# Kernel tuning notes

Measured on AMD Instinct MI355X. Metric: run time of the kernel, lower is better.

## Reference

```python
import jax, jax.numpy as jnp
import numpy as np

D_MODEL = 1024
N_HEADS = 16
HEAD_DIM = D_MODEL // N_HEADS
B, LQ, LK = 2, 2048, 2048
NEG_BIG = -1.0e9


def setup_inputs() -> dict:
    key = jax.random.key(0)
    ks = jax.random.split(key, 12)
    s = 1.0 / np.sqrt(D_MODEL)
    inp = {
        "query": jax.random.normal(ks[0], (B, LQ, D_MODEL), jnp.float32),
        "key": jax.random.normal(ks[1], (B, LK, D_MODEL), jnp.float32),
        "value": jax.random.normal(ks[2], (B, LK, D_MODEL), jnp.float32),
        "mask": jax.random.randint(ks[3], (B, 1, 1, LK), 0, 2, jnp.int32),
        "Wq": jax.random.normal(ks[4], (D_MODEL, D_MODEL), jnp.float32) * s,
        "bq": jnp.zeros((D_MODEL,), jnp.float32),
        "Wk": jax.random.normal(ks[5], (D_MODEL, D_MODEL), jnp.float32) * s,
        "bk": jnp.zeros((D_MODEL,), jnp.float32),
        "Wv": jax.random.normal(ks[6], (D_MODEL, D_MODEL), jnp.float32) * s,
        "bv": jnp.zeros((D_MODEL,), jnp.float32),
        "Wo": jax.random.normal(ks[7], (D_MODEL, D_MODEL), jnp.float32) * s,
        "bo": jnp.zeros((D_MODEL,), jnp.float32),
    }
    return inp


def _split_heads(x):
    # (B, L, E) -> (B, H, L, Dh)
    b, l, _ = x.shape
    return x.reshape(b, l, N_HEADS, HEAD_DIM).transpose(0, 2, 1, 3)


def reference(query, key, value, mask, Wq, bq, Wk, bk, Wv, bv, Wo, bo):
    q = _split_heads(query @ Wq + bq)   # (B,H,Lq,Dh)
    k = _split_heads(key @ Wk + bk)     # (B,H,Lk,Dh)
    v = _split_heads(value @ Wv + bv)   # (B,H,Lk,Dh)

    scale = 1.0 / jnp.sqrt(jnp.asarray(HEAD_DIM, jnp.float32))
    scores = jnp.einsum("bhqd,bhkd->bhqk", q, k) * scale
    scores = scores + mask.astype(scores.dtype) * NEG_BIG
    attn_weights = jax.nn.softmax(scores, axis=-1)  # (B,H,Lq,Lk)
    # dropout in inference mode -> identity
    attn_out = jnp.einsum("bhqk,bhkd->bhqd", attn_weights, v)
    attn_out = attn_out.transpose(0, 2, 1, 3).reshape(B, LQ, D_MODEL)
    out = attn_out @ Wo + bo  # output dropout is identity at inference
    return out, attn_weights
```

## Files before the change

### kernel.cpp

```cpp
#include <hip/hip_runtime.h>


typedef unsigned short u16;
typedef __attribute__((ext_vector_type(8))) short s16x8;
typedef __attribute__((ext_vector_type(8))) unsigned short u16x8;
typedef __attribute__((ext_vector_type(4))) float f32x4;

__device__ __forceinline__ u16 f2b(float f) {
  union { float f; unsigned u; } v; v.f = f;
  return (u16)((v.u + 0x7FFFu + ((v.u >> 16) & 1u)) >> 16);
}

__global__ void cvt_kernel(const float* __restrict__ src, u16* __restrict__ dst, int n8) {
  int i = blockIdx.x * 256 + threadIdx.x;
  if (i >= n8) return;
  typedef __attribute__((ext_vector_type(4))) float f4;
  f4 a = ((const f4*)src)[2 * i];
  f4 b = ((const f4*)src)[2 * i + 1];
  u16x8 o;
  o[0] = f2b(a[0]); o[1] = f2b(a[1]); o[2] = f2b(a[2]); o[3] = f2b(a[3]);
  o[4] = f2b(b[0]); o[5] = f2b(b[1]); o[6] = f2b(b[2]); o[7] = f2b(b[3]);
  ((u16x8*)dst)[i] = o;
}

__global__ void wtrans_kernel(const float* __restrict__ W, u16* __restrict__ Wt) {
  __shared__ float s[64][65];
  int t = threadIdx.x;
  int k0 = blockIdx.x * 64, n0 = blockIdx.y * 64;
#pragma unroll
  for (int i = 0; i < 16; i++) {
    int idx = i * 256 + t;
    int r = idx >> 6, c = idx & 63;
    s[r][c] = W[(size_t)(k0 + r) * 1024 + n0 + c];
  }
  __syncthreads();
#pragma unroll
  for (int i = 0; i < 16; i++) {
    int idx = i * 256 + t;
    int n = idx >> 6, k = idx & 63;
    Wt[(size_t)(n0 + n) * 1024 + k0 + k] = f2b(s[k][n]);
  }
}

__global__ __launch_bounds__(256) void proj_qkv(
    const u16* __restrict__ xq, const u16* __restrict__ xk, const u16* __restrict__ xv,
    const u16* __restrict__ wqt, const u16* __restrict__ wkt, const u16* __restrict__ wvt,
    const float* __restrict__ bqp, const float* __restrict__ bkp, const float* __restrict__ bvp,
    u16* __restrict__ qb, u16* __restrict__ kp, u16* __restrict__ vp) {
  __shared__ u16 lA[128 * 32];
  __shared__ u16 lB[128 * 32];
  int t = threadIdx.x, lane = t & 63, wv = t >> 6;
  int wr = wv >> 1, wc = wv & 1;

  int o = blockIdx.x + (blockIdx.y << 5);
  int wg = (o & 7) * 96 + (o >> 3);
  int mt = wg / 24, y = wg - mt * 24;
  int mode = y >> 3;
  const u16* A = mode == 0 ? xq : mode == 1 ? xk : xv;
  const u16* Bt = mode == 0 ? wqt : mode == 1 ? wkt : wvt;
  const float* bias = mode == 0 ? bqp : mode == 1 ? bkp : bvp;
  int m0 = mt * 128, n0 = (y & 7) * 128;

  f32x4 acc[4][4] = {};

  for (int kt = 0; kt < 1024; kt += 32) {
    __syncthreads();
#pragma unroll
    for (int i = 0; i < 2; i++) {
      int c = wv * 2 + i;
      const u16* ga = A + (size_t)(m0 + c * 16 + (lane >> 2)) * 1024 + kt + (lane & 3) * 8;
      __builtin_amdgcn_global_load_lds((const __attribute__((address_space(1))) void*)ga,
                                       (__attribute__((address_space(3))) void*)&lA[c * 512],
                                       16, 0, 0);
      const u16* gb = Bt + (size_t)(n0 + c * 16 + (lane >> 2)) * 1024 + kt + (lane & 3) * 8;
      __builtin_amdgcn_global_load_lds((const __attribute__((address_space(1))) void*)gb,
                                       (__attribute__((address_space(3))) void*)&lB[c * 512],
                                       16, 0, 0);
    }
    __syncthreads();

    s16x8 af[4], bf[4];
#pragma unroll
    for (int m = 0; m < 4; m++)
      af[m] = *(const s16x8*)&lA[(wr * 64 + m * 16 + (lane & 15)) * 32 + (lane >> 4) * 8];
#pragma unroll
    for (int n = 0; n < 4; n++)
      bf[n] = *(const s16x8*)&lB[(wc * 64 + n * 16 + (lane & 15)) * 32 + (lane >> 4) * 8];
#pragma unroll
    for (int m = 0; m < 4; m++)
#pragma unroll
      for (int n = 0; n < 4; n++)
        acc[m][n] = __builtin_amdgcn_mfma_f32_16x16x32_bf16(af[m], bf[n], acc[m][n], 0, 0, 0);
  }

  float bs[4];
#pragma unroll
  for (int n = 0; n < 4; n++) bs[n] = bias[n0 + wc * 64 + n * 16 + (lane & 15)];

#pragma unroll
  for (int m = 0; m < 4; m++) {
#pragma unroll
    for (int n = 0; n < 4; n++) {
#pragma unroll
      for (int r = 0; r < 4; r++) {
        int row = m0 + wr * 64 + m * 16 + (lane >> 4) * 4 + r;
        int col = n0 + wc * 64 + n * 16 + (lane & 15);
        float v = acc[m][n][r] + bs[n];
        int b = row >> 11, lk = row & 2047, h = col >> 6, d = col & 63;
        size_t bh = (size_t)(b * 16 + h);
        if (mode == 0) {
          qb[((bh * 2048 + lk) << 6) | d] = f2b(v);
        } else if (mode == 1) {
          int tile = lk >> 6, rr = lk & 63, f = rr >> 4;
          int l = (rr & 15) | (((d >> 3) & 3) << 4);
          int kk = d >> 5, e = d & 7;
          kp[(bh << 17) + (tile << 12) + ((kk * 4 + f) << 9) + (l << 3) + e] = f2b(v);
        } else {
          int k = lk, tile = k >> 6, kt_ = k & 63;
          int kk = kt_ >> 5, lhi = (kt_ >> 3) & 3, e = kt_ & 7;
          int n2 = d >> 4, l = (d & 15) | (lhi << 4);
          vp[(bh << 17) + (tile << 12) + ((kk * 4 + n2) << 9) + (l << 3) + e] = f2b(v);
        }
      }
    }
  }
}

__global__ __launch_bounds__(256) void proj_o(const u16* __restrict__ A,
                                              const u16* __restrict__ Bt,
                                              const float* __restrict__ bias,
                                              float* __restrict__ outp) {
  __shared__ u16 lA[128 * 32];
  __shared__ u16 lB[128 * 32];
  int t = threadIdx.x, lane = t & 63, wv = t >> 6;
  int wr = wv >> 1, wc = wv & 1;
  int o = blockIdx.x + (blockIdx.y << 5);
  int wg = ((o & 7) << 5) + (o >> 3);
  int m0 = (wg >> 3) * 128, n0 = (wg & 7) * 128;

  f32x4 acc[4][4] = {};
  for (int kt = 0; kt < 1024; kt += 32) {
    __syncthreads();
#pragma unroll
    for (int i = 0; i < 2; i++) {
      int c = wv * 2 + i;
      const u16* ga = A + (size_t)(m0 + c * 16 + (lane >> 2)) * 1024 + kt + (lane & 3) * 8;
      __builtin_amdgcn_global_load_lds((const __attribute__((address_space(1))) void*)ga,
                                       (__attribute__((address_space(3))) void*)&lA[c * 512],
                                       16, 0, 0);
      const u16* gb = Bt + (size_t)(n0 + c * 16 + (lane >> 2)) * 1024 + kt + (lane & 3) * 8;
      __builtin_amdgcn_global_load_lds((const __attribute__((address_space(1))) void*)gb,
                                       (__attribute__((address_space(3))) void*)&lB[c * 512],
                                       16, 0, 0);
    }
    __syncthreads();

    s16x8 af[4], bf[4];
#pragma unroll
    for (int m = 0; m < 4; m++)
      af[m] = *(const s16x8*)&lA[(wr * 64 + m * 16 + (lane & 15)) * 32 + (lane >> 4) * 8];
#pragma unroll
    for (int n = 0; n < 4; n++)
      bf[n] = *(const s16x8*)&lB[(wc * 64 + n * 16 + (lane & 15)) * 32 + (lane >> 4) * 8];
#pragma unroll
    for (int m = 0; m < 4; m++)
#pragma unroll
      for (int n = 0; n < 4; n++)
        acc[m][n] = __builtin_amdgcn_mfma_f32_16x16x32_bf16(af[m], bf[n], acc[m][n], 0, 0, 0);
  }

  float bs[4];
#pragma unroll
  for (int n = 0; n < 4; n++) bs[n] = bias[n0 + wc * 64 + n * 16 + (lane & 15)];
#pragma unroll
  for (int m = 0; m < 4; m++)
#pragma unroll
    for (int n = 0; n < 4; n++)
#pragma unroll
      for (int r = 0; r < 4; r++) {
        int row = m0 + wr * 64 + m * 16 + (lane >> 4) * 4 + r;
        int col = n0 + wc * 64 + n * 16 + (lane & 15);
        outp[(size_t)row * 1024 + col] = acc[m][n][r] + bs[n];
      }
}

__global__ __launch_bounds__(256) void attn_kernel(
    const u16* __restrict__ qb, const u16* __restrict__ kp, const u16* __restrict__ vp,
    const int* __restrict__ maskg, float* __restrict__ Pout, u16* __restrict__ ao) {
  __shared__ u16 sp[4][16][72];

  int t = threadIdx.x, lane = t & 63, wv = t >> 6;
  int o = blockIdx.x + (blockIdx.y << 5) + (blockIdx.z << 9);
  int wg = ((o & 7) << 7) + (o >> 3);
  int tile = wg & 31, h = (wg >> 5) & 15, b = wg >> 9;

  const u16* qg = qb + (((size_t)(b * 16 + h) * 2048 + tile * 64) << 6);
  const u16* kg = kp + ((size_t)(b * 16 + h) << 17);
  const u16* vg = vp + ((size_t)(b * 16 + h) << 17);
  const int* mg = maskg + (b << 11);
  float* pg = Pout + (((size_t)(b * 16 + h) * 2048 + tile * 64 + wv * 16 + ((lane >> 4) << 2)) << 11) +
              (lane & 15);

  s16x8 af[2];
  {
    const u16* qrow = qg + ((wv * 16 + (lane & 15)) << 6) + ((lane >> 4) << 3);
    af[0] = *(const s16x8*)qrow;
    af[1] = *(const s16x8*)(qrow + 32);
  }

  float s_part[4] = {0.f, 0.f, 0.f, 0.f};
#pragma unroll 1
  for (int kt = 0; kt < 32; kt++) {
    const u16* kb = kg + (kt << 12) + (lane << 3);
    s16x8 kf[8];
#pragma unroll
    for (int i = 0; i < 8; i++) kf[i] = *(const s16x8*)(kb + (i << 9));
    f32x4 sc[4] = {};
#pragma unroll
    for (int kk = 0; kk < 2; kk++)
#pragma unroll
      for (int f = 0; f < 4; f++)
        sc[f] = __builtin_amdgcn_mfma_f32_16x16x32_bf16(af[kk], kf[kk * 4 + f], sc[f], 0, 0, 0);
    float pen[4];
#pragma unroll
    for (int f = 0; f < 4; f++) pen[f] = mg[(kt << 6) + (f << 4) + (lane & 15)] ? -1.0e9f : 0.0f;
#pragma unroll
    for (int r = 0; r < 4; r++) {
      float a = 0.f;
#pragma unroll
      for (int f = 0; f < 4; f++) a += __expf(fmaf(sc[f][r], 0.125f, pen[f]));
      s_part[r] += a;
    }
  }
  float inv[4];
#pragma unroll
  for (int r = 0; r < 4; r++) {
    float a = s_part[r];
#pragma unroll
    for (int d = 1; d < 16; d <<= 1) a += __shfl_xor(a, d);
    inv[r] = 1.0f / a;
  }

  f32x4 oacc[4] = {};
#pragma unroll 1
  for (int kt = 0; kt < 32; kt++) {
    const u16* kb = kg + (kt << 12) + (lane << 3);
    s16x8 kf[8];
#pragma unroll
    for (int i = 0; i < 8; i++) kf[i] = *(const s16x8*)(kb + (i << 9));
    f32x4 sc[4] = {};
#pragma unroll
    for (int kk = 0; kk < 2; kk++)
#pragma unroll
      for (int f = 0; f < 4; f++)
        sc[f] = __builtin_amdgcn_mfma_f32_16x16x32_bf16(af[kk], kf[kk * 4 + f], sc[f], 0, 0, 0);

    const u16* vb = vg + (kt << 12) + (lane << 3);
    s16x8 vf[8];
#pragma unroll
    for (int i = 0; i < 8; i++) vf[i] = *(const s16x8*)(vb + (i << 9));

    float pen[4];
#pragma unroll
    for (int f = 0; f < 4; f++) pen[f] = mg[(kt << 6) + (f << 4) + (lane & 15)] ? -1.0e9f : 0.0f;

#pragma unroll
    for (int f = 0; f < 4; f++) {
#pragma unroll
      for (int r = 0; r < 4; r++) {
        float x = __expf(fmaf(sc[f][r], 0.125f, pen[f])) * inv[r];
        __builtin_nontemporal_store(x, pg + ((size_t)r << 11) + (kt << 6) + (f << 4));
        sp[wv][((lane >> 4) << 2) + r][(f << 4) + (lane & 15)] = f2b(x);
      }
    }
#pragma unroll
    for (int kk = 0; kk < 2; kk++) {
      s16x8 pa = *(const s16x8*)&sp[wv][lane & 15][(kk << 5) + ((lane >> 4) << 3)];
#pragma unroll
      for (int n = 0; n < 4; n++)
        oacc[n] = __builtin_amdgcn_mfma_f32_16x16x32_bf16(pa, vf[kk * 4 + n], oacc[n], 0, 0, 0);
    }
  }

  int qrbase = tile * 64 + wv * 16 + ((lane >> 4) << 2);
#pragma unroll
  for (int n = 0; n < 4; n++)
#pragma unroll
    for (int r = 0; r < 4; r++) {
      int qr = qrbase + r;
      int dc = (h << 6) + (n << 4) + (lane & 15);
      ao[((size_t)(b * 2048 + qr) << 10) + dc] = f2b(oacc[n][r]);
    }
}

extern "C" void kernel_launch(void* const* d_in, const int* in_sizes, int n_in,
                              void* d_out, int out_size, void* d_ws, size_t ws_size,
                              hipStream_t stream) {
  const float* query = (const float*)d_in[0];
  const float* key_ = (const float*)d_in[1];
  const float* value = (const float*)d_in[2];
  const int* mask = (const int*)d_in[3];
  const float* Wq = (const float*)d_in[4];
  const float* bq = (const float*)d_in[5];
  const float* Wk = (const float*)d_in[6];
  const float* bk = (const float*)d_in[7];
  const float* Wv = (const float*)d_in[8];
  const float* bv = (const float*)d_in[9];
  const float* Wo = (const float*)d_in[10];
  const float* bo = (const float*)d_in[11];

  const size_t MB = 1u << 20;
  char* ws = (char*)d_ws;
  u16* xq = (u16*)(ws + 0 * MB);
  u16* xk = (u16*)(ws + 8 * MB);
  u16* xv = (u16*)(ws + 16 * MB);
  u16* wqt = (u16*)(ws + 24 * MB);
  u16* wkt = (u16*)(ws + 26 * MB);
  u16* wvt = (u16*)(ws + 28 * MB);
  u16* wot = (u16*)(ws + 30 * MB);
  u16* qb = (u16*)(ws + 32 * MB);
  u16* kpk = (u16*)(ws + 40 * MB);
  u16* vpk = (u16*)(ws + 48 * MB);
  u16* ao = (u16*)(ws + 56 * MB);

  float* outp = (float*)d_out;
  float* Pout = outp + (size_t)2 * 2048 * 1024;

  cvt_kernel<<<2048, 256, 0, stream>>>(query, xq, 524288);
  cvt_kernel<<<2048, 256, 0, stream>>>(key_, xk, 524288);
  cvt_kernel<<<2048, 256, 0, stream>>>(value, xv, 524288);

  wtrans_kernel<<<dim3(16, 16), 256, 0, stream>>>(Wq, wqt);
  wtrans_kernel<<<dim3(16, 16), 256, 0, stream>>>(Wk, wkt);
  wtrans_kernel<<<dim3(16, 16), 256, 0, stream>>>(Wv, wvt);
  wtrans_kernel<<<dim3(16, 16), 256, 0, stream>>>(Wo, wot);

  proj_qkv<<<dim3(32, 24), 256, 0, stream>>>(xq, xk, xv, wqt, wkt, wvt, bq, bk, bv, qb, kpk, vpk);

  attn_kernel<<<dim3(32, 16, 2), 256, 0, stream>>>(qb, kpk, vpk, mask, Pout, ao);

  proj_o<<<dim3(32, 8), 256, 0, stream>>>(ao, wot, bo, outp);
}
```

Before: 739.4 us.

## Merge prep launches, retile attention and output projection, vectorize probability stores

Folds the three input conversions and four weight transposes into one launch each, and folds the 1/sqrt(d) scale into the Q projection epilogue. The attention kernel now precomputes the mask penalties into shared memory once per block, gives each block 128 query rows processed in two 64-row passes, and stages the fp32 probabilities through shared memory so they go out as 16-byte nontemporal stores instead of scalar stores. The output projection moves to 64x128 tiles with 512 blocks to fill more compute units. The costs are extra shared memory in attention (penalty table plus an fp32 staging tile) and half as many attention blocks, each doing more serial work, which may lower occupancy.

```diff
diff --git a/kernel.cpp b/kernel.cpp
--- a/kernel.cpp
+++ b/kernel.cpp
@@ -5,25 +5,35 @@
 typedef __attribute__((ext_vector_type(8))) short s16x8;
 typedef __attribute__((ext_vector_type(8))) unsigned short u16x8;
 typedef __attribute__((ext_vector_type(4))) float f32x4;
+typedef __attribute__((ext_vector_type(4))) int i32x4;
 
 __device__ __forceinline__ u16 f2b(float f) {
   union { float f; unsigned u; } v; v.f = f;
   return (u16)((v.u + 0x7FFFu + ((v.u >> 16) & 1u)) >> 16);
 }
 
-__global__ void cvt_kernel(const float* __restrict__ src, u16* __restrict__ dst, int n8) {
+__global__ void cvt_all(const float* __restrict__ s0, const float* __restrict__ s1,
+                        const float* __restrict__ s2, u16* __restrict__ d0,
+                        u16* __restrict__ d1, u16* __restrict__ d2) {
+  int y = blockIdx.y;
+  const float* src = y == 0 ? s0 : y == 1 ? s1 : s2;
+  u16* dst = y == 0 ? d0 : y == 1 ? d1 : d2;
   int i = blockIdx.x * 256 + threadIdx.x;
-  if (i >= n8) return;
-  typedef __attribute__((ext_vector_type(4))) float f4;
-  f4 a = ((const f4*)src)[2 * i];
-  f4 b = ((const f4*)src)[2 * i + 1];
+  f32x4 a = ((const f32x4*)src)[2 * i];
+  f32x4 b = ((const f32x4*)src)[2 * i + 1];
   u16x8 o;
   o[0] = f2b(a[0]); o[1] = f2b(a[1]); o[2] = f2b(a[2]); o[3] = f2b(a[3]);
   o[4] = f2b(b[0]); o[5] = f2b(b[1]); o[6] = f2b(b[2]); o[7] = f2b(b[3]);
   ((u16x8*)dst)[i] = o;
 }
 
-__global__ void wtrans_kernel(const float* __restrict__ W, u16* __restrict__ Wt) {
+__global__ void wtrans_all(const float* __restrict__ w0, const float* __restrict__ w1,
+                           const float* __restrict__ w2, const float* __restrict__ w3,
+                           u16* __restrict__ t0, u16* __restrict__ t1,
+                           u16* __restrict__ t2, u16* __restrict__ t3) {
+  int z = blockIdx.z;
+  const float* W = z == 0 ? w0 : z == 1 ? w1 : z == 2 ? w2 : w3;
+  u16* Wt = z == 0 ? t0 : z == 1 ? t1 : z == 2 ? t2 : t3;
   __shared__ float s[64][65];
   int t = threadIdx.x;
   int k0 = blockIdx.x * 64, n0 = blockIdx.y * 64;
@@ -52,7 +62,7 @@
   int t = threadIdx.x, lane = t & 63, wv = t >> 6;
   int wr = wv >> 1, wc = wv & 1;
 
-  int o = blockIdx.x + (blockIdx.y << 5);
+  int o = blockIdx.x;
   int wg = (o & 7) * 96 + (o >> 3);
   int mt = wg / 24, y = wg - mt * 24;
   int mode = y >> 3;
@@ -109,7 +119,7 @@
         int b = row >> 11, lk = row & 2047, h = col >> 6, d = col & 63;
         size_t bh = (size_t)(b * 16 + h);
         if (mode == 0) {
-          qb[((bh * 2048 + lk) << 6) | d] = f2b(v);
+          qb[((bh * 2048 + lk) << 6) | d] = f2b(v * 0.125f);
         } else if (mode == 1) {
           int tile = lk >> 6, rr = lk & 63, f = rr >> 4;
           int l = (rr & 15) | (((d >> 3) & 3) << 4);
@@ -130,56 +140,58 @@
                                               const u16* __restrict__ Bt,
                                               const float* __restrict__ bias,
                                               float* __restrict__ outp) {
-  __shared__ u16 lA[128 * 32];
+  __shared__ u16 lA[64 * 32];
   __shared__ u16 lB[128 * 32];
   int t = threadIdx.x, lane = t & 63, wv = t >> 6;
-  int wr = wv >> 1, wc = wv & 1;
-  int o = blockIdx.x + (blockIdx.y << 5);
-  int wg = ((o & 7) << 5) + (o >> 3);
-  int m0 = (wg >> 3) * 128, n0 = (wg & 7) * 128;
-
-  f32x4 acc[4][4] = {};
+  int o = blockIdx.x;
+  int wg = (o & 7) * 64 + (o >> 3);
+  int m0 = (wg >> 3) * 64, n0 = (wg & 7) * 128;
+
+  f32x4 acc[4][2] = {};
   for (int kt = 0; kt < 1024; kt += 32) {
     __syncthreads();
 #pragma unroll
-    for (int i = 0; i < 2; i++) {
-      int c = wv * 2 + i;
-      const u16* ga = A + (size_t)(m0 + c * 16 + (lane >> 2)) * 1024 + kt + (lane & 3) * 8;
-      __builtin_amdgcn_global_load_lds((const __attribute__((address_space(1))) void*)ga,
-                                       (__attribute__((address_space(3))) void*)&lA[c * 512],
-                                       16, 0, 0);
-      const u16* gb = Bt + (size_t)(n0 + c * 16 + (lane >> 2)) * 1024 + kt + (lane & 3) * 8;
-      __builtin_amdgcn_global_load_lds((const __attribute__((address_space(1))) void*)gb,
-                                       (__attribute__((address_space(3))) void*)&lB[c * 512],
-                                       16, 0, 0);
+    for (int ci = 0; ci < 3; ci++) {
+      int c = wv * 3 + ci;
+      if (c < 4) {
+        const u16* ga = A + (size_t)(m0 + c * 16 + (lane >> 2)) * 1024 + kt + (lane & 3) * 8;
+        __builtin_amdgcn_global_load_lds((const __attribute__((address_space(1))) void*)ga,
+                                         (__attribute__((address_space(3))) void*)&lA[c * 512],
+                                         16, 0, 0);
+      } else {
+        const u16* gb = Bt + (size_t)(n0 + (c - 4) * 16 + (lane >> 2)) * 1024 + kt + (lane & 3) * 8;
+        __builtin_amdgcn_global_load_lds((const __attribute__((address_space(1))) void*)gb,
+                                         (__attribute__((address_space(3))) void*)&lB[(c - 4) * 512],
+                                         16, 0, 0);
+      }
     }
     __syncthreads();
 
-    s16x8 af[4], bf[4];
+    s16x8 af[4], bf[2];
 #pragma unroll
     for (int m = 0; m < 4; m++)
-      af[m] = *(const s16x8*)&lA[(wr * 64 + m * 16 + (lane & 15)) * 32 + (lane >> 4) * 8];
-#pragma unroll
-    for (int n = 0; n < 4; n++)
-      bf[n] = *(const s16x8*)&lB[(wc * 64 + n * 16 + (lane & 15)) * 32 + (lane >> 4) * 8];
+      af[m] = *(const s16x8*)&lA[(m * 16 + (lane & 15)) * 32 + (lane >> 4) * 8];
+#pragma unroll
+    for (int n = 0; n < 2; n++)
+      bf[n] = *(const s16x8*)&lB[(wv * 32 + n * 16 + (lane & 15)) * 32 + (lane >> 4) * 8];
 #pragma unroll
     for (int m = 0; m < 4; m++)
 #pragma unroll
-      for (int n = 0; n < 4; n++)
+      for (int n = 0; n < 2; n++)
         acc[m][n] = __builtin_amdgcn_mfma_f32_16x16x32_bf16(af[m], bf[n], acc[m][n], 0, 0, 0);
   }
 
-  float bs[4];
-#pragma unroll
-  for (int n = 0; n < 4; n++) bs[n] = bias[n0 + wc * 64 + n * 16 + (lane & 15)];
+  float bs[2];
+#pragma unroll
+  for (int n = 0; n < 2; n++) bs[n] = bias[n0 + wv * 32 + n * 16 + (lane & 15)];
 #pragma unroll
   for (int m = 0; m < 4; m++)
 #pragma unroll
-    for (int n = 0; n < 4; n++)
+    for (int n = 0; n < 2; n++)
 #pragma unroll
       for (int r = 0; r < 4; r++) {
-        int row = m0 + wr * 64 + m * 16 + (lane >> 4) * 4 + r;
-        int col = n0 + wc * 64 + n * 16 + (lane & 15);
+        int row = m0 + m * 16 + (lane >> 4) * 4 + r;
+        int col = n0 + wv * 32 + n * 16 + (lane & 15);
         outp[(size_t)row * 1024 + col] = acc[m][n][r] + bs[n];
       }
 }
@@ -187,110 +199,134 @@
 __global__ __launch_bounds__(256) void attn_kernel(
     const u16* __restrict__ qb, const u16* __restrict__ kp, const u16* __restrict__ vp,
     const int* __restrict__ maskg, float* __restrict__ Pout, u16* __restrict__ ao) {
-  __shared__ u16 sp[4][16][72];
+  __shared__ __align__(16) float penl[2048];
+  __shared__ __align__(16) u16 spB[4][16][72];
+  __shared__ __align__(16) float spF[4][16][68];
 
   int t = threadIdx.x, lane = t & 63, wv = t >> 6;
-  int o = blockIdx.x + (blockIdx.y << 5) + (blockIdx.z << 9);
-  int wg = ((o & 7) << 7) + (o >> 3);
-  int tile = wg & 31, h = (wg >> 5) & 15, b = wg >> 9;
-
-  const u16* qg = qb + (((size_t)(b * 16 + h) * 2048 + tile * 64) << 6);
-  const u16* kg = kp + ((size_t)(b * 16 + h) << 17);
-  const u16* vg = vp + ((size_t)(b * 16 + h) << 17);
-  const int* mg = maskg + (b << 11);
-  float* pg = Pout + (((size_t)(b * 16 + h) * 2048 + tile * 64 + wv * 16 + ((lane >> 4) << 2)) << 11) +
-              (lane & 15);
-
-  s16x8 af[2];
+  int lo = lane & 15, hi = lane >> 4;
+  int o = blockIdx.x;
+  int wg = (o & 7) * 64 + (o >> 3);
+  int qp = wg & 15, bh = wg >> 4;
+  int b = bh >> 4, h = bh & 15;
+
+  const u16* qg = qb + (((size_t)bh * 2048 + qp * 128) << 6);
+  const u16* kg = kp + ((size_t)bh << 17);
+  const u16* vg = vp + ((size_t)bh << 17);
+
   {
-    const u16* qrow = qg + ((wv * 16 + (lane & 15)) << 6) + ((lane >> 4) << 3);
-    af[0] = *(const s16x8*)qrow;
-    af[1] = *(const s16x8*)(qrow + 32);
-  }
-
-  float s_part[4] = {0.f, 0.f, 0.f, 0.f};
+    const int* mgp = maskg + (b << 11) + t * 8;
+    i32x4 ma = *(const i32x4*)mgp;
+    i32x4 mb = *(const i32x4*)(mgp + 4);
+    f32x4 pa, pb;
+#pragma unroll
+    for (int j = 0; j < 4; j++) { pa[j] = ma[j] ? -1.0e9f : 0.0f; pb[j] = mb[j] ? -1.0e9f : 0.0f; }
+    *(f32x4*)&penl[t * 8] = pa;
+    *(f32x4*)&penl[t * 8 + 4] = pb;
+  }
+  __syncthreads();
+
 #pragma unroll 1
-  for (int kt = 0; kt < 32; kt++) {
-    const u16* kb = kg + (kt << 12) + (lane << 3);
-    s16x8 kf[8];
-#pragma unroll
-    for (int i = 0; i < 8; i++) kf[i] = *(const s16x8*)(kb + (i << 9));
-    f32x4 sc[4] = {};
-#pragma unroll
-    for (int kk = 0; kk < 2; kk++)
-#pragma unroll
-      for (int f = 0; f < 4; f++)
-        sc[f] = __builtin_amdgcn_mfma_f32_16x16x32_bf16(af[kk], kf[kk * 4 + f], sc[f], 0, 0, 0);
-    float pen[4];
-#pragma unroll
-    for (int f = 0; f < 4; f++) pen[f] = mg[(kt << 6) + (f << 4) + (lane & 15)] ? -1.0e9f : 0.0f;
+  for (int sub = 0; sub < 2; sub++) {
+    s16x8 af[2];
+    {
+      const u16* qrow = qg + ((sub * 64 + wv * 16 + lo) << 6) + (hi << 3);
+      af[0] = *(const s16x8*)qrow;
+      af[1] = *(const s16x8*)(qrow + 32);
+    }
+
+    float s_part[4] = {0.f, 0.f, 0.f, 0.f};
+#pragma unroll 1
+    for (int kt = 0; kt < 32; kt++) {
+      const u16* kb = kg + (kt << 12) + (lane << 3);
+      s16x8 kf[8];
+#pragma unroll
+      for (int i = 0; i < 8; i++) kf[i] = *(const s16x8*)(kb + (i << 9));
+      f32x4 sc[4] = {};
+#pragma unroll
+      for (int kk = 0; kk < 2; kk++)
+#pragma unroll
+        for (int f = 0; f < 4; f++)
+          sc[f] = __builtin_amdgcn_mfma_f32_16x16x32_bf16(af[kk], kf[kk * 4 + f], sc[f], 0, 0, 0);
+      float pe[4];
+#pragma unroll
+      for (int f = 0; f < 4; f++) pe[f] = penl[(kt << 6) + (f << 4) + lo];
+#pragma unroll
+      for (int r = 0; r < 4; r++) {
+        float a = 0.f;
+#pragma unroll
+        for (int f = 0; f < 4; f++) a += __expf(sc[f][r] + pe[f]);
+        s_part[r] += a;
+      }
+    }
+    float inv[4];
 #pragma unroll
     for (int r = 0; r < 4; r++) {
-      float a = 0.f;
-#pragma unroll
-      for (int f = 0; f < 4; f++) a += __expf(fmaf(sc[f][r], 0.125f, pen[f]));
-      s_part[r] += a;
-    }
-  }
-  float inv[4];
-#pragma unroll
-  for (int r = 0; r < 4; r++) {
-    float a = s_part[r];
-#pragma unroll
-    for (int d = 1; d < 16; d <<= 1) a += __shfl_xor(a, d);
-    inv[r] = 1.0f / a;
-  }
-
-  f32x4 oacc[4] = {};
+      float a = s_part[r];
+#pragma unroll
+      for (int d = 1; d < 16; d <<= 1) a += __shfl_xor(a, d);
+      inv[r] = 1.0f / a;
+    }
+
+    float* Pg = Pout + (((size_t)bh * 2048 + qp * 128 + sub * 64 + wv * 16) << 11);
+    f32x4 oacc[4] = {};
 #pragma unroll 1
-  for (int kt = 0; kt < 32; kt++) {
-    const u16* kb = kg + (kt << 12) + (lane << 3);
-    s16x8 kf[8];
-#pragma unroll
-    for (int i = 0; i < 8; i++) kf[i] = *(const s16x8*)(kb + (i << 9));
-    f32x4 sc[4] = {};
-#pragma unroll
-    for (int kk = 0; kk < 2; kk++)
-#pragma unroll
-      for (int f = 0; f < 4; f++)
-        sc[f] = __builtin_amdgcn_mfma_f32_16x16x32_bf16(af[kk], kf[kk * 4 + f], sc[f], 0, 0, 0);
-
-    const u16* vb = vg + (kt << 12) + (lane << 3);
-    s16x8 vf[8];
-#pragma unroll
-    for (int i = 0; i < 8; i++) vf[i] = *(const s16x8*)(vb + (i << 9));
-
-    float pen[4];
-#pragma unroll
-    for (int f = 0; f < 4; f++) pen[f] = mg[(kt << 6) + (f << 4) + (lane & 15)] ? -1.0e9f : 0.0f;
-
-#pragma unroll
-    for (int f = 0; f < 4; f++) {
+    for (int kt = 0; kt < 32; kt++) {
+      const u16* kb = kg + (kt << 12) + (lane << 3);
+      s16x8 kf[8];
+#pragma unroll
+      for (int i = 0; i < 8; i++) kf[i] = *(const s16x8*)(kb + (i << 9));
+      f32x4 sc[4] = {};
+#pragma unroll
+      for (int kk = 0; kk < 2; kk++)
+#pragma unroll
+        for (int f = 0; f < 4; f++)
+          sc[f] = __builtin_amdgcn_mfma_f32_16x16x32_bf16(af[kk], kf[kk * 4 + f], sc[f], 0, 0, 0);
+
+      const u16* vb = vg + (kt << 12) + (lane << 3);
+      s16x8 vf[8];
+#pragma unroll
+      for (int i = 0; i < 8; i++) vf[i] = *(const s16x8*)(vb + (i << 9));
+
+      float pe[4];
+#pragma unroll
+      for (int f = 0; f < 4; f++) pe[f] = penl[(kt << 6) + (f << 4) + lo];
+
+#pragma unroll
+      for (int f = 0; f < 4; f++) {
+#pragma unroll
+        for (int r = 0; r < 4; r++) {
+          float x = __expf(sc[f][r] + pe[f]) * inv[r];
+          int qr = (hi << 2) + r;
+          spB[wv][qr][(f << 4) + lo] = f2b(x);
+          spF[wv][qr][(f << 4) + lo] = x;
+        }
+      }
+#pragma unroll
+      for (int kk = 0; kk < 2; kk++) {
+        s16x8 pa = *(const s16x8*)&spB[wv][lo][(kk << 5) + (hi << 3)];
+#pragma unroll
+        for (int n = 0; n < 4; n++)
+          oacc[n] = __builtin_amdgcn_mfma_f32_16x16x32_bf16(pa, vf[kk * 4 + n], oacc[n], 0, 0, 0);
+      }
+#pragma unroll
+      for (int i = 0; i < 4; i++) {
+        f32x4 pv = *(const f32x4*)&spF[wv][(i << 2) + hi][lo << 2];
+        float* addr = Pg + (((size_t)(i << 2) + hi) << 11) + (kt << 6) + (lo << 2);
+        __builtin_nontemporal_store(pv, (f32x4*)addr);
+      }
+    }
+
+    int qrbase = qp * 128 + sub * 64 + wv * 16 + (hi << 2);
+#pragma unroll
+    for (int n = 0; n < 4; n++)
 #pragma unroll
       for (int r = 0; r < 4; r++) {
-        float x = __expf(fmaf(sc[f][r], 0.125f, pen[f])) * inv[r];
-        __builtin_nontemporal_store(x, pg + ((size_t)r << 11) + (kt << 6) + (f << 4));
-        sp[wv][((lane >> 4) << 2) + r][(f << 4) + (lane & 15)] = f2b(x);
-      }
-    }
-#pragma unroll
-    for (int kk = 0; kk < 2; kk++) {
-      s16x8 pa = *(const s16x8*)&sp[wv][lane & 15][(kk << 5) + ((lane >> 4) << 3)];
-#pragma unroll
-      for (int n = 0; n < 4; n++)
-        oacc[n] = __builtin_amdgcn_mfma_f32_16x16x32_bf16(pa, vf[kk * 4 + n], oacc[n], 0, 0, 0);
-    }
-  }
-
-  int qrbase = tile * 64 + wv * 16 + ((lane >> 4) << 2);
-#pragma unroll
-  for (int n = 0; n < 4; n++)
-#pragma unroll
-    for (int r = 0; r < 4; r++) {
-      int qr = qrbase + r;
-      int dc = (h << 6) + (n << 4) + (lane & 15);
-      ao[((size_t)(b * 2048 + qr) << 10) + dc] = f2b(oacc[n][r]);
-    }
+        int qr = qrbase + r;
+        int dc = (h << 6) + (n << 4) + lo;
+        ao[((size_t)(b * 2048 + qr) << 10) + dc] = f2b(oacc[n][r]);
+      }
+  }
 }
 
 extern "C" void kernel_launch(void* const* d_in, const int* in_sizes, int n_in,
@@ -318,7 +354,7 @@
   u16* wkt = (u16*)(ws + 26 * MB);
   u16* wvt = (u16*)(ws + 28 * MB);
   u16* wot = (u16*)(ws + 30 * MB);
-  u16* qb = (u16*)(ws + 32 * MB);
+  u16* qbuf = (u16*)(ws + 32 * MB);
   u16* kpk = (u16*)(ws + 40 * MB);
   u16* vpk = (u16*)(ws + 48 * MB);
   u16* ao = (u16*)(ws + 56 * MB);
@@ -326,18 +362,9 @@
   float* outp = (float*)d_out;
   float* Pout = outp + (size_t)2 * 2048 * 1024;
 
-  cvt_kernel<<<2048, 256, 0, stream>>>(query, xq, 524288);
-  cvt_kernel<<<2048, 256, 0, stream>>>(key_, xk, 524288);
-  cvt_kernel<<<2048, 256, 0, stream>>>(value, xv, 524288);
-
-  wtrans_kernel<<<dim3(16, 16), 256, 0, stream>>>(Wq, wqt);
-  wtrans_kernel<<<dim3(16, 16), 256, 0, stream>>>(Wk, wkt);
-  wtrans_kernel<<<dim3(16, 16), 256, 0, stream>>>(Wv, wvt);
-  wtrans_kernel<<<dim3(16, 16), 256, 0, stream>>>(Wo, wot);
-
-  proj_qkv<<<dim3(32, 24), 256, 0, stream>>>(xq, xk, xv, wqt, wkt, wvt, bq, bk, bv, qb, kpk, vpk);
-
-  attn_kernel<<<dim3(32, 16, 2), 256, 0, stream>>>(qb, kpk, vpk, mask, Pout, ao);
-
-  proj_o<<<dim3(32, 8), 256, 0, stream>>>(ao, wot, bo, outp);
-}
+  cvt_all<<<dim3(2048, 3), 256, 0, stream>>>(query, key_, value, xq, xk, xv);
+  wtrans_all<<<dim3(16, 16, 4), 256, 0, stream>>>(Wq, Wk, Wv, Wo, wqt, wkt, wvt, wot);
+  proj_qkv<<<768, 256, 0, stream>>>(xq, xk, xv, wqt, wkt, wvt, bq, bk, bv, qbuf, kpk, vpk);
+  attn_kernel<<<512, 256, 0, stream>>>(qbuf, kpk, vpk, mask, Pout, ao);
+  proj_o<<<512, 256, 0, stream>>>(ao, wot, bo, outp);
+}
```

Measured after the change: 732.3 us. Within noise of the previous version (-1.0%).
